# Kernel tuning notes

Hardware: AMD Instinct MI355X
Metric: run time of the kernel (lower is better)

## Reference

```python
import jax, jax.numpy as jnp
import numpy as np

B, T, NN = 128, 128, 8          # batch, time_window, nodes per graph (hardcoded in source)
N = B * T * NN                  # 131072 flattened node rows
F_IN, C = 32, 64                # node_features, spatial_features
E = 1_048_576                   # edges (avg degree 8)
EPS = 1e-5


def _gcn(x, src, dst, W, b):
    # PyG GCNConv: h = D^{-1/2}(A+I)D^{-1/2} X W + b, self-loops added, symmetric norm
    h = x @ W                                           # [N, C]
    loop = jnp.arange(N, dtype=src.dtype)
    s = jnp.concatenate([src, loop])
    d = jnp.concatenate([dst, loop])
    deg = jax.ops.segment_sum(jnp.ones_like(s, dtype=h.dtype), d, num_segments=N)
    dinv = jax.lax.rsqrt(deg)                           # deg >= 1 due to self loops
    msg = h[s] * (dinv[s] * dinv[d])[:, None]           # gather + scale
    out = jax.ops.segment_sum(msg, d, num_segments=N)   # scatter-add
    return out + b


def _conv2d(x, w, b, pad_w):
    y = jax.lax.conv_general_dilated(
        x, w, window_strides=(1, 1), padding=[(0, 0), (pad_w, pad_w)],
        dimension_numbers=("NCHW", "OIHW", "NCHW"))
    return y + b[None, :, None, None]


def _bn_relu(x, g, beta):
    # BatchNorm2d in training mode: batch statistics, biased variance
    mu = x.mean(axis=(0, 2, 3), keepdims=True)
    var = x.var(axis=(0, 2, 3), keepdims=True)
    y = (x - mu) * jax.lax.rsqrt(var + EPS)
    return jax.nn.relu(y * g[None, :, None, None] + beta[None, :, None, None])


def _layer(x, src, dst, gw, gb, tw, tb, bg, bb, ow, ob):
    h = _gcn(x, src, dst, gw, gb)                       # [N, C]
    h = h.reshape(B, T, NN, -1).transpose(0, 3, 2, 1)   # [B, C, NN, T]
    h = _conv2d(h, tw, tb, 1)                           # (1,3) temporal conv, pad (0,1)
    h = _bn_relu(h, bg, bb)
    h = _conv2d(h, ow, ob, 0)                           # 1x1 conv (squeeze() is a no-op here)
    h = jnp.tanh(h)
    return h.reshape(-1, h.shape[1])                    # faithful to x.view(-1, x.shape[1])


def setup_inputs() -> dict:
    key = jax.random.key(0)
    ks = jax.random.split(key, 20)
    p = lambda k, shape: (jax.random.normal(k, shape, jnp.float32) * 0.05)
    inp = {
        "x": jax.random.normal(ks[0], (N, F_IN), jnp.float32),
        "edge_index": jax.random.randint(ks[1], (2, E), 0, N, jnp.int32),
        "gcn1_w": p(ks[2], (F_IN, C)), "gcn1_b": jnp.zeros((C,), jnp.float32),
        "t1_w": p(ks[3], (C, C, 1, 3)), "t1_b": jnp.zeros((C,), jnp.float32),
        "bn1_g": jnp.ones((C,), jnp.float32), "bn1_b": jnp.zeros((C,), jnp.float32),
        "o1_w": p(ks[4], (C, C, 1, 1)), "o1_b": jnp.zeros((C,), jnp.float32),
        "gcn2_w": p(ks[5], (C, C)), "gcn2_b": jnp.zeros((C,), jnp.float32),
        "t2_w": p(ks[6], (C, C, 1, 3)), "t2_b": jnp.zeros((C,), jnp.float32),
        "bn2_g": jnp.ones((C,), jnp.float32), "bn2_b": jnp.zeros((C,), jnp.float32),
        "o2_w": p(ks[7], (C, C, 1, 1)), "o2_b": jnp.zeros((C,), jnp.float32),
        "reg_w": p(ks[8], (C, 8)), "reg_b": jnp.zeros((8,), jnp.float32),
    }
    return inp


def reference(x, edge_index, gcn1_w, gcn1_b, t1_w, t1_b, bn1_g, bn1_b, o1_w, o1_b,
              gcn2_w, gcn2_b, t2_w, t2_b, bn2_g, bn2_b, o2_w, o2_b, reg_w, reg_b):
    src, dst = edge_index[0], edge_index[1]
    h = _layer(x, src, dst, gcn1_w, gcn1_b, t1_w, t1_b, bn1_g, bn1_b, o1_w, o1_b)
    h = _layer(h, src, dst, gcn2_w, gcn2_b, t2_w, t2_b, bn2_g, bn2_b, o2_w, o2_b)
    h = h @ reg_w + reg_b                                # [N, 8]
    h = h.reshape(B, T, NN, -1)
    return h.mean(axis=(1, 3))                           # [B, NN] = [128, 8]
```

## Files before the change

### kernel.cpp

```cpp
#include <hip/hip_runtime.h>
#include <stdint.h>

typedef unsigned short u16;
typedef __attribute__((ext_vector_type(8))) short bf16x8;
typedef __attribute__((ext_vector_type(4))) float f32x4;

static const int N_NODES = 131072;
static const int N_EDGES = 1048576;

__device__ __forceinline__ float u2f(u16 u){
  union{uint32_t i; float f;} w; w.i = ((uint32_t)u)<<16; return w.f;
}
__device__ __forceinline__ u16 f2u(float f){
  union{float f; uint32_t u;} v; v.f=f;
  uint32_t u=v.u;
  u += 0x7fff + ((u>>16)&1);
  return (u16)(u>>16);
}
__device__ __forceinline__ float bits2f(uint32_t b){
  union{uint32_t i; float f;} w; w.i = b; return w.f;
}
__device__ __forceinline__ float ldv(const float* p, int i){ return p[i]; }
__device__ __forceinline__ float ldv(const u16* p, int i){ return u2f(p[i]); }
__device__ __forceinline__ void stv(float* p, int i, float v){ p[i]=v; }
__device__ __forceinline__ void stv(u16* p, int i, float v){ p[i]=f2u(v); }
__device__ __forceinline__ float ldmix(const void* p, int i, int isbf){
  return isbf ? u2f(((const u16*)p)[i]) : ((const float*)p)[i];
}

__global__ __launch_bounds__(256) void k_detect(const uint32_t* __restrict__ x, int* __restrict__ flag,
                                                float* __restrict__ stats1, float* __restrict__ stats2,
                                                float* __restrict__ zacc){
  int tid = threadIdx.x;
  if (tid < 128){ stats1[tid] = 0.f; stats2[tid] = 0.f; }
  for (int i=tid; i<1024; i+=256) zacc[i] = 0.f;
  if (tid == 0){
    int cnt=0;
    for (int i=0;i<256;i++){
      uint32_t e=(x[i]>>7)&0xFFu;
      if (e>=0x6Fu && e<=0x85u) cnt++;
    }
    *flag = (cnt>=128) ? 1 : 0;
  }
}

__global__ __launch_bounds__(256) void k_hist(const int* __restrict__ dst, int* __restrict__ H){
  __shared__ int h[256];
  int tid = threadIdx.x;
  h[tid] = 0;
  __syncthreads();
  int base = blockIdx.x*4096;
  #pragma unroll
  for (int i=0;i<16;i++){
    int e = base + i*256 + tid;
    atomicAdd(&h[(dst[e] & (N_NODES-1))>>9], 1);
  }
  __syncthreads();
  H[blockIdx.x*256 + tid] = h[tid];
}

__global__ __launch_bounds__(256) void k_colscan(const int* __restrict__ H, int* __restrict__ P,
                                                 int* __restrict__ bt){
  __shared__ int sc[256];
  int b = blockIdx.x, tid = threadIdx.x;
  int v = H[tid*256 + b];
  sc[tid] = v; __syncthreads();
  for (int d=1; d<256; d<<=1){
    int o = (tid>=d) ? sc[tid-d] : 0; __syncthreads();
    sc[tid] += o; __syncthreads();
  }
  P[tid*256 + b] = sc[tid] - v;
  if (tid==255) bt[b] = sc[255];
}

__global__ __launch_bounds__(256) void k_scatter2(const int* __restrict__ src, const int* __restrict__ dst,
                                                  const int* __restrict__ P, const int* __restrict__ bt,
                                                  uint32_t* __restrict__ ebuf){
  __shared__ int cu[256], sc[256];
  int tid = threadIdx.x;
  int v = bt[tid];
  sc[tid] = v; __syncthreads();
  for (int d=1; d<256; d<<=1){
    int o = (tid>=d) ? sc[tid-d] : 0; __syncthreads();
    sc[tid] += o; __syncthreads();
  }
  cu[tid] = (sc[tid] - v) + P[blockIdx.x*256 + tid];
  __syncthreads();
  int base = blockIdx.x*4096;
  #pragma unroll
  for (int i=0;i<16;i++){
    int e = base + i*256 + tid;
    int s = src[e] & (N_NODES-1);
    int d = dst[e] & (N_NODES-1);
    int pos = atomicAdd(&cu[d>>9], 1);
    ebuf[pos] = (uint32_t)s | ((uint32_t)(d & 511) << 17);
  }
}

__global__ __launch_bounds__(512) void k_bsort2(const uint32_t* __restrict__ ebuf, const int* __restrict__ bt,
                                                const void* __restrict__ x, const int* __restrict__ flag,
                                                int* __restrict__ adj, int* __restrict__ offs,
                                                int* __restrict__ deg, float* __restrict__ dinv,
                                                u16* __restrict__ Bout){
  __shared__ uint32_t ein[5120], outs[5120];
  __shared__ int hist[512], sc[512], cu[512];
  __shared__ int sct[256];
  __shared__ float dv[512];
  int b = blockIdx.x, tid = threadIdx.x;
  if (tid < 256){ sct[tid] = bt[tid]; }
  __syncthreads();
  for (int d=1; d<256; d<<=1){
    int o = (tid < 256 && tid>=d) ? sct[tid-d] : 0; __syncthreads();
    if (tid < 256) sct[tid] += o; __syncthreads();
  }
  int lo = sct[b] - bt[b], hi = sct[b];
  int cnt = hi - lo; if (cnt > 5120) cnt = 5120; if (cnt < 0) cnt = 0;
  hist[tid] = 0;
  __syncthreads();
  for (int i=tid; i<cnt; i+=512){
    uint32_t p = ebuf[lo+i];
    ein[i] = p;
    atomicAdd(&hist[(p>>17)&511], 1);
  }
  __syncthreads();
  sc[tid] = hist[tid];
  __syncthreads();
  for (int d=1; d<512; d<<=1){
    int v = (tid>=d) ? sc[tid-d] : 0;
    __syncthreads();
    sc[tid] += v;
    __syncthreads();
  }
  {
    int ex = sc[tid] - hist[tid];
    int node = b*512 + tid;
    offs[node] = lo + ex;
    deg[node]  = hist[tid];
    float rs = rsqrtf((float)hist[tid] + 1.0f);
    dinv[node] = rs;
    dv[tid] = rs;
    cu[tid] = ex;
  }
  __syncthreads();
  for (int i=tid; i<cnt; i+=512){
    uint32_t p = ein[i];
    int pos = atomicAdd(&cu[(p>>17)&511], 1);
    outs[pos] = p & 0x1FFFFu;
  }
  __syncthreads();
  for (int i=tid; i<cnt; i+=512) adj[lo+i] = (int)outs[i];
  int isbf = *flag;
  for (int u=tid; u<16384; u+=512){
    int nl = u>>5, c = u&31;
    int idx = ((b<<9) + nl)*32 + c;
    stv(Bout, idx, dv[nl]*ldmix(x, idx, isbf));
  }
}

__device__ __forceinline__ void acc16(uint4 a, float* acc){
  acc[0] += bits2f(a.x<<16); acc[1] += bits2f(a.x&0xFFFF0000u);
  acc[2] += bits2f(a.y<<16); acc[3] += bits2f(a.y&0xFFFF0000u);
  acc[4] += bits2f(a.z<<16); acc[5] += bits2f(a.z&0xFFFF0000u);
  acc[6] += bits2f(a.w<<16); acc[7] += bits2f(a.w&0xFFFF0000u);
}
template<int F>
__global__ __launch_bounds__(256) void k_aggp2(const u16* __restrict__ Xs,
                                               const int* __restrict__ adj, const int* __restrict__ offs,
                                               const int* __restrict__ deg, const float* __restrict__ dinv,
                                               u16* __restrict__ out){
  constexpr int CH  = F/8;
  constexpr int GPW = 64/CH;
  int tid = threadIdx.x;
  int wv = tid>>6, lane = tid&63;
  int g = lane / CH;
  int k = lane % CH;
  int n = blockIdx.x*(4*GPW) + wv*GPW + g;
  int o = offs[n] & (N_EDGES-1);
  int cnt = min(deg[n], 8192);
  const uint4* X4 = (const uint4*)Xs;
  uint4 sv = X4[(size_t)n*CH + k];
  float acc[8] = {0,0,0,0,0,0,0,0};
  acc16(sv, acc);
  int e = 0;
  for (; e+8 <= cnt; e += 8){
    int i0 = adj[o+e+0] & (N_NODES-1);
    int i1 = adj[o+e+1] & (N_NODES-1);
    int i2 = adj[o+e+2] & (N_NODES-1);
    int i3 = adj[o+e+3] & (N_NODES-1);
    int i4 = adj[o+e+4] & (N_NODES-1);
    int i5 = adj[o+e+5] & (N_NODES-1);
    int i6 = adj[o+e+6] & (N_NODES-1);
    int i7 = adj[o+e+7] & (N_NODES-1);
    uint4 a0 = X4[(size_t)i0*CH + k];
    uint4 a1 = X4[(size_t)i1*CH + k];
    uint4 a2 = X4[(size_t)i2*CH + k];
    uint4 a3 = X4[(size_t)i3*CH + k];
    uint4 a4 = X4[(size_t)i4*CH + k];
    uint4 a5 = X4[(size_t)i5*CH + k];
    uint4 a6 = X4[(size_t)i6*CH + k];
    uint4 a7 = X4[(size_t)i7*CH + k];
    acc16(a0, acc); acc16(a1, acc); acc16(a2, acc); acc16(a3, acc);
    acc16(a4, acc); acc16(a5, acc); acc16(a6, acc); acc16(a7, acc);
  }
  if (e+4 <= cnt){
    int i0 = adj[o+e+0] & (N_NODES-1);
    int i1 = adj[o+e+1] & (N_NODES-1);
    int i2 = adj[o+e+2] & (N_NODES-1);
    int i3 = adj[o+e+3] & (N_NODES-1);
    uint4 a0 = X4[(size_t)i0*CH + k];
    uint4 a1 = X4[(size_t)i1*CH + k];
    uint4 a2 = X4[(size_t)i2*CH + k];
    uint4 a3 = X4[(size_t)i3*CH + k];
    acc16(a0, acc); acc16(a1, acc); acc16(a2, acc); acc16(a3, acc);
    e += 4;
  }
  for (; e < cnt; e++){
    int s = adj[o+e] & (N_NODES-1);
    uint4 a = X4[(size_t)s*CH + k];
    acc16(a, acc);
  }
  float dv = dinv[n];
  uint4 r;
  r.x = (uint32_t)f2u(acc[0]*dv) | ((uint32_t)f2u(acc[1]*dv) << 16);
  r.y = (uint32_t)f2u(acc[2]*dv) | ((uint32_t)f2u(acc[3]*dv) << 16);
  r.z = (uint32_t)f2u(acc[4]*dv) | ((uint32_t)f2u(acc[5]*dv) << 16);
  r.w = (uint32_t)f2u(acc[6]*dv) | ((uint32_t)f2u(acc[7]*dv) << 16);
  ((uint4*)out)[(size_t)n*CH + k] = r;
}

__device__ __forceinline__ void wcomb_one(int Kin, const void* gW, const void* gb, const void* tw,
                                          int isbf, u16* Wtb, float* braw, int r, int co){
  if (r < 3*Kin){
    int k = r / Kin, j = r - (r/Kin)*Kin;
    float acc = 0.f;
    for (int c=0; c<64; c++)
      acc += ldmix(gW, j*64+c, isbf) * ldmix(tw, co*192 + c*3 + k, isbf);
    Wtb[co*(3*Kin) + r] = f2u(acc);
  } else {
    int k = r - 3*Kin;
    float acc = 0.f;
    for (int c=0; c<64; c++)
      acc += ldmix(gb, c, isbf) * ldmix(tw, co*192 + c*3 + k, isbf);
    braw[k*64 + co] = acc;
  }
}
__global__ __launch_bounds__(64) void k_wcombB(const void* __restrict__ g1w, const void* __restrict__ g1b,
                                               const void* __restrict__ t1w,
                                               const void* __restrict__ g2w, const void* __restrict__ g2b,
                                               const void* __restrict__ t2w,
                                               const void* __restrict__ o1w, const void* __restrict__ o2w,
                                               const int* __restrict__ flag,
                                               u16* __restrict__ Wtb1, float* __restrict__ braw1,
                                               u16* __restrict__ Wtb2, float* __restrict__ braw2,
                                               u16* __restrict__ owb1, u16* __restrict__ owb2){
  int isbf = *flag;
  int r = blockIdx.x, co = threadIdx.x;
  if (r < 99) wcomb_one(32, g1w, g1b, t1w, isbf, Wtb1, braw1, r, co);
  else if (r < 294) wcomb_one(64, g2w, g2b, t2w, isbf, Wtb2, braw2, r-99, co);
  else if (r < 358){
    int row = r - 294;
    owb1[row*64 + co] = f2u(ldmix(o1w, row*64 + co, isbf));
  } else {
    int row = r - 358;
    owb2[row*64 + co] = f2u(ldmix(o2w, row*64 + co, isbf));
  }
}

template<int Kin>
__global__ __launch_bounds__(256) void k_tconv3(const u16* __restrict__ A, const u16* __restrict__ Wtb,
                                                const float* __restrict__ braw, const void* __restrict__ tb,
                                                const int* __restrict__ flag, u16* __restrict__ out,
                                                float* __restrict__ stats){
  constexpr int K  = 3*Kin;
  constexpr int SA = Kin + 8;
  constexpr int JH = Kin/2;
  constexpr int JL = (Kin==64) ? 5 : 4;
  __shared__ alignas(16) u16 At[130*SA];
  __shared__ float ball[64], bs0[64], bs2[64];
  __shared__ float wsum[4][64], wsum2[4][64];

  int isbf = *flag;
  int bid = blockIdx.x;
  int b = bid>>3, v = bid&7;
  const int tid = threadIdx.x;

  if (tid < 64){
    float b0=braw[tid], b1=braw[64+tid], b2=braw[128+tid];
    ball[tid] = ldmix(tb, tid, isbf) + b0 + b1 + b2;
    bs0[tid] = b0; bs2[tid] = b2;
  }
  {
    uint32_t* Ad = (uint32_t*)At;
    const uint32_t* Ag = (const uint32_t*)A;
    for (int u=tid; u<130*JH; u+=256){
      int t1 = u >> JL, jd = u & (JH-1);
      int t = t1 - 1;
      uint32_t pack = 0;
      if (t >= 0 && t < 128)
        pack = Ag[((((b*128+t)*8+v))*Kin >> 1) + jd];
      Ad[t1*(SA/2) + jd] = pack;
    }
  }
  __syncthreads();

  int wv_ = tid >> 6, lane = tid & 63;
  int q = lane >> 4, l16 = lane & 15;
  int tb0 = wv_ * 32;

  f32x4 acc[2][4];
  #pragma unroll
  for (int mt=0; mt<2; mt++)
    #pragma unroll
    for (int nt=0; nt<4; nt++)
      acc[mt][nt] = (f32x4){0.f,0.f,0.f,0.f};

  #pragma unroll
  for (int s=0; s<K/32; s++){
    int kk = (32*s)/Kin;
    int j0 = 32*s - kk*Kin;
    int col = j0 + q*8;
    bf16x8 afr[2], bfr[4];
    #pragma unroll
    for (int mt=0; mt<2; mt++){
      int row = tb0 + mt*16 + l16 + kk;
      afr[mt] = *(const bf16x8*)&At[row*SA + col];
    }
    #pragma unroll
    for (int nt=0; nt<4; nt++){
      int co = nt*16 + l16;
      bfr[nt] = *(const bf16x8*)&Wtb[co*K + 32*s + q*8];
    }
    #pragma unroll
    for (int mt=0; mt<2; mt++)
      #pragma unroll
      for (int nt=0; nt<4; nt++)
        acc[mt][nt] = __builtin_amdgcn_mfma_f32_16x16x32_bf16(afr[mt], bfr[nt], acc[mt][nt], 0, 0, 0);
  }

  float ls[4] = {0,0,0,0}, ls2[4] = {0,0,0,0};
  #pragma unroll
  for (int mt=0; mt<2; mt++){
    #pragma unroll
    for (int r=0; r<4; r++){
      int t = tb0 + mt*16 + q*4 + r;
      int base = (((b*128+t)*8+v)) << 6;
      #pragma unroll
      for (int nt=0; nt<4; nt++){
        int co = nt*16 + l16;
        float val = acc[mt][nt][r] + ball[co];
        if (t == 0)   val -= bs0[co];
        if (t == 127) val -= bs2[co];
        out[base + co] = f2u(val);
        ls[nt] += val; ls2[nt] += val*val;
      }
    }
  }
  #pragma unroll
  for (int nt=0; nt<4; nt++){
    ls[nt]  += __shfl_xor(ls[nt], 16);  ls[nt]  += __shfl_xor(ls[nt], 32);
    ls2[nt] += __shfl_xor(ls2[nt], 16); ls2[nt] += __shfl_xor(ls2[nt], 32);
  }
  if (q == 0){
    #pragma unroll
    for (int nt=0; nt<4; nt++){
      wsum[wv_][nt*16 + l16]  = ls[nt];
      wsum2[wv_][nt*16 + l16] = ls2[nt];
    }
  }
  __syncthreads();
  if (tid < 64){
    float a = wsum[0][tid]+wsum[1][tid]+wsum[2][tid]+wsum[3][tid];
    float a2 = wsum2[0][tid]+wsum2[1][tid]+wsum2[2][tid]+wsum2[3][tid];
    atomicAdd(&stats[tid], a);
    atomicAdd(&stats[64+tid], a2);
  }
}

template<bool FINAL>
__global__ __launch_bounds__(256) void k_bnfuse3(const u16* __restrict__ X, const float* __restrict__ stats,
                                                 const void* __restrict__ gam, const void* __restrict__ bet,
                                                 const u16* __restrict__ owb, const void* __restrict__ ob,
                                                 const int* __restrict__ flag, const float* __restrict__ presc,
                                                 u16* __restrict__ out16,
                                                 float* __restrict__ zacc, const void* __restrict__ rw){
  constexpr int SA = 72;
  __shared__ alignas(16) u16 Yl[128*SA];
  __shared__ float kk[64], bsh[64], obs[64];
  __shared__ float rw_s[64];
  __shared__ float wred[4];
  int isbf = *flag;
  int bid = blockIdx.x;
  int b = bid>>3, v = bid&7;
  const int tid = threadIdx.x;
  const float invM = 1.0f/131072.0f;

  if (tid < 64){
    int ci = tid;
    float mu = stats[ci]*invM;
    float var = stats[64+ci]*invM - mu*mu;
    float rs = rsqrtf(fmaxf(var, 0.f) + 1e-5f);
    float kv = rs*ldmix(gam, ci, isbf);
    kk[ci] = kv;
    bsh[ci] = ldmix(bet, ci, isbf) - mu*kv;
    obs[ci] = ldmix(ob, ci, isbf);
    if (FINAL){
      float s = 0.f;
      #pragma unroll
      for (int f=0; f<8; f++) s += ldmix(rw, ci*8 + f, isbf);
      rw_s[ci] = s;
    }
  }
  __syncthreads();
  {
    uint32_t* Yd = (uint32_t*)Yl;
    const uint32_t* Xg = (const uint32_t*)X;
    for (int u=tid; u<128*32; u+=256){
      int t = u>>5, jd = u&31;
      int ci = jd<<1;
      int rowbase = (((b*128+t)*8+v)) << 6;
      uint32_t pr = Xg[(rowbase>>1) + jd];
      float x0 = bits2f(pr<<16);
      float x1 = bits2f(pr & 0xFFFF0000u);
      float y0 = fmaxf(x0*kk[ci] + bsh[ci], 0.f);
      float y1 = fmaxf(x1*kk[ci+1] + bsh[ci+1], 0.f);
      Yd[t*(SA/2) + jd] = (uint32_t)f2u(y0) | ((uint32_t)f2u(y1) << 16);
    }
  }
  __syncthreads();

  int wv_ = tid >> 6, lane = tid & 63;
  int q = lane >> 4, l16 = lane & 15;
  int tb0 = wv_ * 32;

  f32x4 acc[2][4];
  #pragma unroll
  for (int mt=0; mt<2; mt++)
    #pragma unroll
    for (int nt=0; nt<4; nt++)
      acc[mt][nt] = (f32x4){0.f,0.f,0.f,0.f};

  #pragma unroll
  for (int s=0; s<2; s++){
    int col = 32*s + q*8;
    bf16x8 afr[2], bfr[4];
    #pragma unroll
    for (int mt=0; mt<2; mt++){
      int row = tb0 + mt*16 + l16;
      afr[mt] = *(const bf16x8*)&Yl[row*SA + col];
    }
    #pragma unroll
    for (int nt=0; nt<4; nt++){
      int co = nt*16 + l16;
      bfr[nt] = *(const bf16x8*)&owb[co*64 + col];
    }
    #pragma unroll
    for (int mt=0; mt<2; mt++)
      #pragma unroll
      for (int nt=0; nt<4; nt++)
        acc[mt][nt] = __builtin_amdgcn_mfma_f32_16x16x32_bf16(afr[mt], bfr[nt], acc[mt][nt], 0, 0, 0);
  }

  __syncthreads();
  #pragma unroll
  for (int mt=0; mt<2; mt++){
    #pragma unroll
    for (int r=0; r<4; r++){
      int t = tb0 + mt*16 + q*4 + r;
      #pragma unroll
      for (int nt=0; nt<4; nt++){
        int co = nt*16 + l16;
        Yl[t*SA + co] = f2u(acc[mt][nt][r] + obs[co]);
      }
    }
  }
  __syncthreads();
  if (!FINAL){
    for (int u=tid; u<8192; u+=256){
      int l = u & 63;
      int idx = u >> 6;
      int co = idx >> 1, thi = idx & 1;
      int t = (thi<<6) + l;
      float z = tanhf(u2f(Yl[t*SA + co]));
      int r = (b<<10) + (co<<4) + (v<<1) + thi;
      if (presc) z *= presc[r];
      out16[(r<<6) + l] = f2u(z);
    }
  } else {
    float zsum = 0.f;
    for (int u=tid; u<8192; u+=256){
      int l = u & 63;
      int idx = u >> 6;
      int co = idx >> 1;
      int t = ((idx & 1)<<6) + l;
      float z = tanhf(u2f(Yl[t*SA + co]));
      zsum += z * rw_s[l];
    }
    for (int off=32; off; off>>=1) zsum += __shfl_down(zsum, off);
    if (lane == 0) wred[wv_] = zsum;
    __syncthreads();
    if (tid == 0){
      int base = (b<<3) + ((v&3)<<1);
      atomicAdd(&zacc[base],   wred[0] + wred[2]);
      atomicAdd(&zacc[base+1], wred[1] + wred[3]);
    }
  }
}

__global__ __launch_bounds__(256) void k_fin2(const float* __restrict__ zacc, const void* __restrict__ rb,
                                              const int* __restrict__ flag, void* __restrict__ out){
  int i = blockIdx.x*256 + threadIdx.x;
  if (i >= 1024) return;
  int isbf = *flag;
  float rbs = 0.f;
  #pragma unroll
  for (int f=0; f<8; f++) rbs += ldmix(rb, f, isbf);
  float val = zacc[i]*(1.0f/1024.0f) + rbs*0.125f;
  if (isbf) ((u16*)out)[i] = f2u(val);
  else      ((float*)out)[i] = val;
}

extern "C" void kernel_launch(void* const* d_in, const int* in_sizes, int n_in,
                              void* d_out, int out_size, void* d_ws, size_t ws_size,
                              hipStream_t stream){
  (void)in_sizes; (void)n_in; (void)out_size; (void)ws_size;
  char* p = (char*)d_ws;
  auto alloc = [&](size_t bytes){ void* r = (void*)p; p += (bytes + 255) & ~(size_t)255; return r; };
  u16*   U1   = (u16*)  alloc(sizeof(u16)*(size_t)N_NODES*64);
  u16*   U2   = (u16*)  alloc(sizeof(u16)*(size_t)N_NODES*64);
  u16*   C16  = (u16*)  alloc(sizeof(u16)*(size_t)N_NODES*64);
  int*   deg  = (int*)  alloc(sizeof(int)*N_NODES);
  float* dinv = (float*)alloc(sizeof(float)*N_NODES);
  int*   offs = (int*)  alloc(sizeof(int)*N_NODES);
  int*   adj  = (int*)  alloc(sizeof(int)*N_EDGES);
  int*   H    = (int*)  alloc(sizeof(int)*256*256);
  int*   P    = (int*)  alloc(sizeof(int)*256*256);
  int*   bt   = (int*)  alloc(sizeof(int)*256);
  float* stats1=(float*)alloc(sizeof(float)*128);
  float* stats2=(float*)alloc(sizeof(float)*128);
  int*   flag = (int*)  alloc(sizeof(int)*64);
  u16*   Wtb1 = (u16*)  alloc(sizeof(u16)*96*64);
  float* braw1= (float*)alloc(sizeof(float)*192);
  u16*   Wtb2 = (u16*)  alloc(sizeof(u16)*192*64);
  float* braw2= (float*)alloc(sizeof(float)*192);
  u16*   owb1 = (u16*)  alloc(sizeof(u16)*64*64);
  u16*   owb2 = (u16*)  alloc(sizeof(u16)*64*64);
  float* zacc = (float*)alloc(sizeof(float)*1024);
  uint32_t* ebuf = (uint32_t*)C16;
  u16* Bs16 = U1;
  u16* A16  = U1 + (size_t)N_NODES*32;
  u16* D16  = U1;
  u16* E16  = U2;

  const void* x   = d_in[0];
  const int* edge = (const int*)d_in[1];
  const void* g1w = d_in[2];  const void* g1b = d_in[3];
  const void* t1w = d_in[4];  const void* t1b = d_in[5];
  const void* bn1g= d_in[6];  const void* bn1b= d_in[7];
  const void* o1w = d_in[8];  const void* o1b = d_in[9];
  const void* g2w = d_in[10]; const void* g2b = d_in[11];
  const void* t2w = d_in[12]; const void* t2b = d_in[13];
  const void* bn2g= d_in[14]; const void* bn2b= d_in[15];
  const void* o2w = d_in[16]; const void* o2b = d_in[17];
  const void* rw  = d_in[18]; const void* rb  = d_in[19];
  const int* src = edge;
  const int* dst = edge + N_EDGES;

  k_detect<<<1, 256, 0, stream>>>((const uint32_t*)x, flag, stats1, stats2, zacc);

  k_hist    <<<256, 256, 0, stream>>>(dst, H);
  k_colscan <<<256, 256, 0, stream>>>(H, P, bt);
  k_scatter2<<<256, 256, 0, stream>>>(src, dst, P, bt, ebuf);
  k_bsort2  <<<256, 512, 0, stream>>>(ebuf, bt, x, flag, adj, offs, deg, dinv, Bs16);

  k_wcombB<<<422, 64, 0, stream>>>(g1w, g1b, t1w, g2w, g2b, t2w, o1w, o2w, flag,
                                   Wtb1, braw1, Wtb2, braw2, owb1, owb2);

  k_aggp2<32>  <<<N_NODES/64, 256, 0, stream>>>(Bs16, adj, offs, deg, dinv, A16);
  k_tconv3<32> <<<1024, 256, 0, stream>>>(A16, Wtb1, braw1, t1b, flag, C16, stats1);
  k_bnfuse3<false><<<1024, 256, 0, stream>>>(C16, stats1, bn1g, bn1b, owb1, o1b, flag, dinv, D16,
                                             (float*)nullptr, (const void*)nullptr);

  k_aggp2<64>  <<<N_NODES/32, 256, 0, stream>>>(D16, adj, offs, deg, dinv, E16);
  k_tconv3<64> <<<1024, 256, 0, stream>>>(E16, Wtb2, braw2, t2b, flag, C16, stats2);
  k_bnfuse3<true><<<1024, 256, 0, stream>>>(C16, stats2, bn2g, bn2b, owb2, o2b, flag, (const float*)nullptr,
                                            (u16*)nullptr, zacc, rw);
  k_fin2<<<4, 256, 0, stream>>>(zacc, rb, flag, d_out);
}
```

Before: 316.3 us.

## Split tconv and bnfuse blocks by time halves and bank BN stat atomics

Measured after the change: 299.6 us. -5.3%, faster.

```diff
diff --git a/kernel.cpp b/kernel.cpp
--- a/kernel.cpp
+++ b/kernel.cpp
@@ -32,7 +32,7 @@
                                                 float* __restrict__ stats1, float* __restrict__ stats2,
                                                 float* __restrict__ zacc){
   int tid = threadIdx.x;
-  if (tid < 128){ stats1[tid] = 0.f; stats2[tid] = 0.f; }
+  for (int i=tid; i<512; i+=256){ stats1[i] = 0.f; stats2[i] = 0.f; }
   for (int i=tid; i<1024; i+=256) zacc[i] = 0.f;
   if (tid == 0){
     int cnt=0;
@@ -275,13 +275,13 @@
   constexpr int SA = Kin + 8;
   constexpr int JH = Kin/2;
   constexpr int JL = (Kin==64) ? 5 : 4;
-  __shared__ alignas(16) u16 At[130*SA];
+  __shared__ alignas(16) u16 At[66*SA];
   __shared__ float ball[64], bs0[64], bs2[64];
   __shared__ float wsum[4][64], wsum2[4][64];
 
   int isbf = *flag;
   int bid = blockIdx.x;
-  int b = bid>>3, v = bid&7;
+  int b = bid>>4, rem = bid&15, v = rem>>1, th = rem&1;
   const int tid = threadIdx.x;
 
   if (tid < 64){
@@ -292,87 +292,76 @@
   {
     uint32_t* Ad = (uint32_t*)At;
     const uint32_t* Ag = (const uint32_t*)A;
-    for (int u=tid; u<130*JH; u+=256){
-      int t1 = u >> JL, jd = u & (JH-1);
-      int t = t1 - 1;
+    for (int u=tid; u<66*JH; u+=256){
+      int ls = u >> JL, jd = u & (JH-1);
+      int t = th*64 + ls - 1;
       uint32_t pack = 0;
       if (t >= 0 && t < 128)
         pack = Ag[((((b*128+t)*8+v))*Kin >> 1) + jd];
-      Ad[t1*(SA/2) + jd] = pack;
+      Ad[ls*(SA/2) + jd] = pack;
     }
   }
   __syncthreads();
 
   int wv_ = tid >> 6, lane = tid & 63;
   int q = lane >> 4, l16 = lane & 15;
-  int tb0 = wv_ * 32;
-
-  f32x4 acc[2][4];
-  #pragma unroll
-  for (int mt=0; mt<2; mt++)
-    #pragma unroll
-    for (int nt=0; nt<4; nt++)
-      acc[mt][nt] = (f32x4){0.f,0.f,0.f,0.f};
+  int ltb0 = wv_ * 16;
+
+  f32x4 acc[4];
+  #pragma unroll
+  for (int nt=0; nt<4; nt++) acc[nt] = (f32x4){0.f,0.f,0.f,0.f};
 
   #pragma unroll
   for (int s=0; s<K/32; s++){
     int kk = (32*s)/Kin;
     int j0 = 32*s - kk*Kin;
     int col = j0 + q*8;
-    bf16x8 afr[2], bfr[4];
-    #pragma unroll
-    for (int mt=0; mt<2; mt++){
-      int row = tb0 + mt*16 + l16 + kk;
-      afr[mt] = *(const bf16x8*)&At[row*SA + col];
-    }
+    bf16x8 afr = *(const bf16x8*)&At[(ltb0 + l16 + kk)*SA + col];
+    bf16x8 bfr[4];
     #pragma unroll
     for (int nt=0; nt<4; nt++){
       int co = nt*16 + l16;
       bfr[nt] = *(const bf16x8*)&Wtb[co*K + 32*s + q*8];
     }
     #pragma unroll
-    for (int mt=0; mt<2; mt++)
-      #pragma unroll
-      for (int nt=0; nt<4; nt++)
-        acc[mt][nt] = __builtin_amdgcn_mfma_f32_16x16x32_bf16(afr[mt], bfr[nt], acc[mt][nt], 0, 0, 0);
-  }
-
-  float ls[4] = {0,0,0,0}, ls2[4] = {0,0,0,0};
-  #pragma unroll
-  for (int mt=0; mt<2; mt++){
-    #pragma unroll
-    for (int r=0; r<4; r++){
-      int t = tb0 + mt*16 + q*4 + r;
-      int base = (((b*128+t)*8+v)) << 6;
-      #pragma unroll
-      for (int nt=0; nt<4; nt++){
-        int co = nt*16 + l16;
-        float val = acc[mt][nt][r] + ball[co];
-        if (t == 0)   val -= bs0[co];
-        if (t == 127) val -= bs2[co];
-        out[base + co] = f2u(val);
-        ls[nt] += val; ls2[nt] += val*val;
-      }
+    for (int nt=0; nt<4; nt++)
+      acc[nt] = __builtin_amdgcn_mfma_f32_16x16x32_bf16(afr, bfr[nt], acc[nt], 0, 0, 0);
+  }
+
+  float ls_[4] = {0,0,0,0}, ls2_[4] = {0,0,0,0};
+  #pragma unroll
+  for (int r=0; r<4; r++){
+    int t = th*64 + ltb0 + q*4 + r;
+    int base = (((b*128+t)*8+v)) << 6;
+    #pragma unroll
+    for (int nt=0; nt<4; nt++){
+      int co = nt*16 + l16;
+      float val = acc[nt][r] + ball[co];
+      if (t == 0)   val -= bs0[co];
+      if (t == 127) val -= bs2[co];
+      out[base + co] = f2u(val);
+      ls_[nt] += val; ls2_[nt] += val*val;
     }
   }
   #pragma unroll
   for (int nt=0; nt<4; nt++){
-    ls[nt]  += __shfl_xor(ls[nt], 16);  ls[nt]  += __shfl_xor(ls[nt], 32);
-    ls2[nt] += __shfl_xor(ls2[nt], 16); ls2[nt] += __shfl_xor(ls2[nt], 32);
+    ls_[nt]  += __shfl_xor(ls_[nt], 16);  ls_[nt]  += __shfl_xor(ls_[nt], 32);
+    ls2_[nt] += __shfl_xor(ls2_[nt], 16); ls2_[nt] += __shfl_xor(ls2_[nt], 32);
   }
   if (q == 0){
     #pragma unroll
     for (int nt=0; nt<4; nt++){
-      wsum[wv_][nt*16 + l16]  = ls[nt];
-      wsum2[wv_][nt*16 + l16] = ls2[nt];
+      wsum[wv_][nt*16 + l16]  = ls_[nt];
+      wsum2[wv_][nt*16 + l16] = ls2_[nt];
     }
   }
   __syncthreads();
   if (tid < 64){
     float a = wsum[0][tid]+wsum[1][tid]+wsum[2][tid]+wsum[3][tid];
     float a2 = wsum2[0][tid]+wsum2[1][tid]+wsum2[2][tid]+wsum2[3][tid];
-    atomicAdd(&stats[tid], a);
-    atomicAdd(&stats[64+tid], a2);
+    int bank = (bid & 3) * 128;
+    atomicAdd(&stats[bank + tid], a);
+    atomicAdd(&stats[bank + 64 + tid], a2);
   }
 }
 
@@ -384,20 +373,22 @@
                                                  u16* __restrict__ out16,
                                                  float* __restrict__ zacc, const void* __restrict__ rw){
   constexpr int SA = 72;
-  __shared__ alignas(16) u16 Yl[128*SA];
+  __shared__ alignas(16) u16 Yl[64*SA];
   __shared__ float kk[64], bsh[64], obs[64];
   __shared__ float rw_s[64];
   __shared__ float wred[4];
   int isbf = *flag;
   int bid = blockIdx.x;
-  int b = bid>>3, v = bid&7;
+  int b = bid>>4, rem = bid&15, v = rem>>1, th = rem&1;
   const int tid = threadIdx.x;
   const float invM = 1.0f/131072.0f;
 
   if (tid < 64){
     int ci = tid;
-    float mu = stats[ci]*invM;
-    float var = stats[64+ci]*invM - mu*mu;
+    float s1 = stats[ci] + stats[128+ci] + stats[256+ci] + stats[384+ci];
+    float s2 = stats[64+ci] + stats[192+ci] + stats[320+ci] + stats[448+ci];
+    float mu = s1*invM;
+    float var = s2*invM - mu*mu;
     float rs = rsqrtf(fmaxf(var, 0.f) + 1e-5f);
     float kv = rs*ldmix(gam, ci, isbf);
     kk[ci] = kv;
@@ -414,94 +405,78 @@
   {
     uint32_t* Yd = (uint32_t*)Yl;
     const uint32_t* Xg = (const uint32_t*)X;
-    for (int u=tid; u<128*32; u+=256){
-      int t = u>>5, jd = u&31;
+    for (int u=tid; u<64*32; u+=256){
+      int lt = u>>5, jd = u&31;
       int ci = jd<<1;
+      int t = th*64 + lt;
       int rowbase = (((b*128+t)*8+v)) << 6;
       uint32_t pr = Xg[(rowbase>>1) + jd];
       float x0 = bits2f(pr<<16);
       float x1 = bits2f(pr & 0xFFFF0000u);
       float y0 = fmaxf(x0*kk[ci] + bsh[ci], 0.f);
       float y1 = fmaxf(x1*kk[ci+1] + bsh[ci+1], 0.f);
-      Yd[t*(SA/2) + jd] = (uint32_t)f2u(y0) | ((uint32_t)f2u(y1) << 16);
+      Yd[lt*(SA/2) + jd] = (uint32_t)f2u(y0) | ((uint32_t)f2u(y1) << 16);
     }
   }
   __syncthreads();
 
   int wv_ = tid >> 6, lane = tid & 63;
   int q = lane >> 4, l16 = lane & 15;
-  int tb0 = wv_ * 32;
-
-  f32x4 acc[2][4];
-  #pragma unroll
-  for (int mt=0; mt<2; mt++)
-    #pragma unroll
-    for (int nt=0; nt<4; nt++)
-      acc[mt][nt] = (f32x4){0.f,0.f,0.f,0.f};
+  int ltb0 = wv_ * 16;
+
+  f32x4 acc[4];
+  #pragma unroll
+  for (int nt=0; nt<4; nt++) acc[nt] = (f32x4){0.f,0.f,0.f,0.f};
 
   #pragma unroll
   for (int s=0; s<2; s++){
     int col = 32*s + q*8;
-    bf16x8 afr[2], bfr[4];
-    #pragma unroll
-    for (int mt=0; mt<2; mt++){
-      int row = tb0 + mt*16 + l16;
-      afr[mt] = *(const bf16x8*)&Yl[row*SA + col];
-    }
+    bf16x8 afr = *(const bf16x8*)&Yl[(ltb0 + l16)*SA + col];
+    bf16x8 bfr[4];
     #pragma unroll
     for (int nt=0; nt<4; nt++){
       int co = nt*16 + l16;
       bfr[nt] = *(const bf16x8*)&owb[co*64 + col];
     }
     #pragma unroll
-    for (int mt=0; mt<2; mt++)
-      #pragma unroll
-      for (int nt=0; nt<4; nt++)
-        acc[mt][nt] = __builtin_amdgcn_mfma_f32_16x16x32_bf16(afr[mt], bfr[nt], acc[mt][nt], 0, 0, 0);
-  }
-
-  __syncthreads();
-  #pragma unroll
-  for (int mt=0; mt<2; mt++){
-    #pragma unroll
-    for (int r=0; r<4; r++){
-      int t = tb0 + mt*16 + q*4 + r;
-      #pragma unroll
-      for (int nt=0; nt<4; nt++){
-        int co = nt*16 + l16;
-        Yl[t*SA + co] = f2u(acc[mt][nt][r] + obs[co]);
-      }
+    for (int nt=0; nt<4; nt++)
+      acc[nt] = __builtin_amdgcn_mfma_f32_16x16x32_bf16(afr, bfr[nt], acc[nt], 0, 0, 0);
+  }
+
+  __syncthreads();
+  #pragma unroll
+  for (int r=0; r<4; r++){
+    int lt = ltb0 + q*4 + r;
+    #pragma unroll
+    for (int nt=0; nt<4; nt++){
+      int co = nt*16 + l16;
+      Yl[lt*SA + co] = f2u(acc[nt][r] + obs[co]);
     }
   }
   __syncthreads();
   if (!FINAL){
-    for (int u=tid; u<8192; u+=256){
+    for (int u=tid; u<4096; u+=256){
       int l = u & 63;
-      int idx = u >> 6;
-      int co = idx >> 1, thi = idx & 1;
-      int t = (thi<<6) + l;
-      float z = tanhf(u2f(Yl[t*SA + co]));
-      int r = (b<<10) + (co<<4) + (v<<1) + thi;
+      int co = u >> 6;
+      float z = tanhf(u2f(Yl[l*SA + co]));
+      int r = (b<<10) + (co<<4) + (v<<1) + th;
       if (presc) z *= presc[r];
       out16[(r<<6) + l] = f2u(z);
     }
   } else {
     float zsum = 0.f;
-    for (int u=tid; u<8192; u+=256){
+    for (int u=tid; u<4096; u+=256){
       int l = u & 63;
-      int idx = u >> 6;
-      int co = idx >> 1;
-      int t = ((idx & 1)<<6) + l;
-      float z = tanhf(u2f(Yl[t*SA + co]));
+      int co = u >> 6;
+      float z = tanhf(u2f(Yl[l*SA + co]));
       zsum += z * rw_s[l];
     }
     for (int off=32; off; off>>=1) zsum += __shfl_down(zsum, off);
     if (lane == 0) wred[wv_] = zsum;
     __syncthreads();
     if (tid == 0){
-      int base = (b<<3) + ((v&3)<<1);
-      atomicAdd(&zacc[base],   wred[0] + wred[2]);
-      atomicAdd(&zacc[base+1], wred[1] + wred[3]);
+      int base = (b<<3) + ((v&3)<<1) + th;
+      atomicAdd(&zacc[base], wred[0] + wred[1] + wred[2] + wred[3]);
     }
   }
 }
@@ -535,8 +510,8 @@
   int*   H    = (int*)  alloc(sizeof(int)*256*256);
   int*   P    = (int*)  alloc(sizeof(int)*256*256);
   int*   bt   = (int*)  alloc(sizeof(int)*256);
-  float* stats1=(float*)alloc(sizeof(float)*128);
-  float* stats2=(float*)alloc(sizeof(float)*128);
+  float* stats1=(float*)alloc(sizeof(float)*512);
+  float* stats2=(float*)alloc(sizeof(float)*512);
   int*   flag = (int*)  alloc(sizeof(int)*64);
   u16*   Wtb1 = (u16*)  alloc(sizeof(u16)*96*64);
   float* braw1= (float*)alloc(sizeof(float)*192);
@@ -576,13 +551,13 @@
                                    Wtb1, braw1, Wtb2, braw2, owb1, owb2);
 
   k_aggp2<32>  <<<N_NODES/64, 256, 0, stream>>>(Bs16, adj, offs, deg, dinv, A16);
-  k_tconv3<32> <<<1024, 256, 0, stream>>>(A16, Wtb1, braw1, t1b, flag, C16, stats1);
-  k_bnfuse3<false><<<1024, 256, 0, stream>>>(C16, stats1, bn1g, bn1b, owb1, o1b, flag, dinv, D16,
+  k_tconv3<32> <<<2048, 256, 0, stream>>>(A16, Wtb1, braw1, t1b, flag, C16, stats1);
+  k_bnfuse3<false><<<2048, 256, 0, stream>>>(C16, stats1, bn1g, bn1b, owb1, o1b, flag, dinv, D16,
                                              (float*)nullptr, (const void*)nullptr);
 
   k_aggp2<64>  <<<N_NODES/32, 256, 0, stream>>>(D16, adj, offs, deg, dinv, E16);
-  k_tconv3<64> <<<1024, 256, 0, stream>>>(E16, Wtb2, braw2, t2b, flag, C16, stats2);
-  k_bnfuse3<true><<<1024, 256, 0, stream>>>(C16, stats2, bn2g, bn2b, owb2, o2b, flag, (const float*)nullptr,
+  k_tconv3<64> <<<2048, 256, 0, stream>>>(E16, Wtb2, braw2, t2b, flag, C16, stats2);
+  k_bnfuse3<true><<<2048, 256, 0, stream>>>(C16, stats2, bn2g, bn2b, owb2, o2b, flag, (const float*)nullptr,
                                             (u16*)nullptr, zacc, rw);
   k_fin2<<<4, 256, 0, stream>>>(zacc, rb, flag, d_out);
 }
```
